# Kernel tuning notes

Measured on AMD Instinct MI355X. Metric: run time of the kernel, lower is better.

The kernel has to match this reference:

```python
import jax, jax.numpy as jnp
import numpy as np


def _dequantize(qweight, scale, zero_point, bits, group_size):
    """Unpack int32-packed weights and apply group-wise dequantization.

    qweight:    [N, K // (32//bits)] int32, value i within an int32 at shift i*bits
    scale/zp:   [N, K // group_size]
    returns W:  [N, K] float32
    """
    vpi = 32 // bits  # values per int32
    mask = (1 << bits) - 1
    N, packed = qweight.shape
    K = packed * vpi
    shifts = (jnp.arange(vpi, dtype=jnp.int32) * bits)  # [vpi]
    # [N, packed, vpi] -> flatten so value i of each int32 lands at consecutive K positions
    q = (qweight[:, :, None] >> shifts[None, None, :]) & mask
    q = q.reshape(N, K // group_size, group_size).astype(jnp.float32)
    w = scale[:, :, None] * (q - zero_point[:, :, None])  # group-wise dequant
    return w.reshape(N, K)


def setup_inputs() -> dict:
    key = jax.random.key(0)
    k1, k2, k3, k4, k5 = jax.random.split(key, 5)
    B, S, K, N = 4, 2048, 4096, 4096
    bits, group_size = 4, 128
    vpi = 32 // bits
    num_groups = K // group_size
    x = jax.random.normal(k1, (B, S, K), dtype=jnp.float32)
    qweight = jax.random.randint(k2, (N, K // vpi), jnp.iinfo(jnp.int32).min,
                                 jnp.iinfo(jnp.int32).max, dtype=jnp.int32)
    scale = jax.random.uniform(k3, (N, num_groups), dtype=jnp.float32,
                               minval=0.001, maxval=0.02)
    zero_point = jax.random.uniform(k4, (N, num_groups), dtype=jnp.float32,
                                    minval=0.0, maxval=float((1 << bits) - 1))
    bias = jax.random.normal(k5, (N,), dtype=jnp.float32)
    return {"x": x, "qweight": qweight, "scale": scale, "zero_point": zero_point,
            "bias": bias, "bits": bits, "group_size": group_size}


def reference(x, qweight, scale, zero_point, bias, bits, group_size):
    # Fused dequant + GEMM: y = x @ W^T + b, W dequantized from packed int4 groups
    w = _dequantize(qweight, scale, zero_point, bits, group_size)  # [N, K]
    y = jnp.einsum('bsk,nk->bsn', x, w)
    return y + bias
```

## Files before the change

### kernel.cpp

```cpp
#include <hip/hip_runtime.h>

#define KD 4096
#define ND 4096
#define GRP 32
#define NT (KD / 64)

typedef unsigned short u16;
typedef float   f32x4  __attribute__((ext_vector_type(4)));
typedef __bf16  bf16x8 __attribute__((ext_vector_type(8)));
typedef unsigned short u16x8 __attribute__((ext_vector_type(8)));
typedef unsigned short u16x4 __attribute__((ext_vector_type(4)));

__device__ __forceinline__ u16 f2bf(float f) {
  unsigned u = __float_as_uint(f);
  return (u16)((u + 0x7fffu + ((u >> 16) & 1u)) >> 16);
}

__device__ __forceinline__ void async16(const void* g, void* l) {
  __builtin_amdgcn_global_load_lds(
      (const __attribute__((address_space(1))) unsigned int*)g,
      (__attribute__((address_space(3))) unsigned int*)l, 16, 0, 0);
}

__global__ __launch_bounds__(256) void prep_kernel(
    const int* __restrict__ qw, const float* __restrict__ scale,
    const float* __restrict__ zp, u16* __restrict__ wout,
    const float4* __restrict__ x, u16x4* __restrict__ xb, int nx) {
  const int nth = gridDim.x * 256;
  const int t0 = blockIdx.x * 256 + threadIdx.x;
  for (int idx = t0; idx < ND * (KD / 8); idx += nth) {
    int n = idx >> 9;
    int p = idx & 511;
    int g = p >> 4;
    float s = scale[n * GRP + g];
    float bz = -s * zp[n * GRP + g];
    unsigned q = (unsigned)qw[idx];
    u16x8 hv;
#pragma unroll
    for (int i = 0; i < 8; ++i)
      hv[i] = f2bf(fmaf((float)((q >> (4 * i)) & 15u), s, bz));
    *(u16x8*)(wout + (size_t)idx * 8) = hv;
  }
  for (int i = t0; i < nx; i += nth) {
    float4 v = x[i];
    u16x4 h;
    h[0] = f2bf(v.x); h[1] = f2bf(v.y); h[2] = f2bf(v.z); h[3] = f2bf(v.w);
    xb[i] = h;
  }
}

__global__ __launch_bounds__(512, 2) void gemm256(
    const u16* __restrict__ xb, const u16* __restrict__ wb,
    const float* __restrict__ bias, float* __restrict__ out) {
  __shared__ u16 As[2][256 * 64];
  __shared__ u16 Bs[2][256 * 64];
  const int tid = threadIdx.x;
  const int l = tid & 63, w = tid >> 6;
  const int wr = w >> 2, wc = w & 3;
  const int col = l & 15, quad = l >> 4, rsw = col & 7;
  const int lr = l >> 3, csrc = (l & 7) ^ lr;

  const int id = blockIdx.y * gridDim.x + blockIdx.x;
  const int nwg = gridDim.x * gridDim.y;
  const int q = nwg >> 3, r = nwg & 7;
  const int xcd = id & 7, off = id >> 3;
  const int wgid = (xcd < r ? xcd * (q + 1) : r * (q + 1) + (xcd - r) * q) + off;
  const int nb = gridDim.x;
  const int m0 = (wgid / nb) * 256;
  const int n0 = (wgid % nb) * 256;

  const u16* asrc = xb + (size_t)(m0 + w * 16 + lr) * KD + csrc * 8;
  const u16* bsrc = wb + (size_t)(n0 + w * 16 + lr) * KD + csrc * 8;

#define STAGE_A(t, h)                                                      \
  do {                                                                     \
    const u16* _g = asrc + (size_t)((h) * 128) * KD + (t) * 64;            \
    u16* _l = &As[(t) & 1][((h) * 128 + w * 16) * 64];                     \
    async16(_g, _l);                                                       \
    async16(_g + (size_t)8 * KD, _l + 8 * 64);                             \
  } while (0)
#define STAGE_B(t, h)                                                      \
  do {                                                                     \
    const u16* _g = bsrc + (size_t)((h) * 128) * KD + (t) * 64;            \
    u16* _l = &Bs[(t) & 1][((h) * 128 + w * 16) * 64];                     \
    async16(_g, _l);                                                       \
    async16(_g + (size_t)8 * KD, _l + 8 * 64);                             \
  } while (0)
#define BAR()   __builtin_amdgcn_s_barrier()
#define SB0()   __builtin_amdgcn_sched_barrier(0)
#define LGKM0() do { asm volatile("s_waitcnt lgkmcnt(0)"); SB0(); } while (0)
#define LDA(Ab, i, kk) \
  (*(const bf16x8*)&(Ab)[(wr * 128 + (i) * 16 + col) * 64 + ((((kk) * 4 + quad) ^ rsw) * 8)])
#define LDB(Bb, j, kk) \
  (*(const bf16x8*)&(Bb)[(wc * 64 + (j) * 16 + col) * 64 + ((((kk) * 4 + quad) ^ rsw) * 8)])

  f32x4 acc[8][4] = {};
  bf16x8 a[4][2], b[4][2];

  STAGE_A(0, 0); STAGE_A(0, 1); STAGE_B(0, 0); STAGE_B(0, 1);
  STAGE_B(1, 0); STAGE_B(1, 1);
  asm volatile("s_waitcnt vmcnt(4)");
  SB0();
  BAR();

  for (int t = 0; t < NT; ++t) {
    const u16* Ab = As[t & 1];
    const u16* Bb = Bs[t & 1];

#pragma unroll
    for (int i = 0; i < 4; ++i) { a[i][0] = LDA(Ab, i, 0); a[i][1] = LDA(Ab, i, 1); }
#pragma unroll
    for (int j = 0; j < 2; ++j) { b[j][0] = LDB(Bb, j, 0); b[j][1] = LDB(Bb, j, 1); }
    if (t + 1 < NT) STAGE_A(t + 1, 0);
    BAR();
    LGKM0();
    __builtin_amdgcn_s_setprio(1);
#pragma unroll
    for (int kk = 0; kk < 2; ++kk)
#pragma unroll
      for (int i = 0; i < 4; ++i)
#pragma unroll
        for (int j = 0; j < 2; ++j)
          acc[i][j] = __builtin_amdgcn_mfma_f32_16x16x32_bf16(a[i][kk], b[j][kk], acc[i][j], 0, 0, 0);
    __builtin_amdgcn_s_setprio(0);
    BAR();

#pragma unroll
    for (int j = 2; j < 4; ++j) { b[j][0] = LDB(Bb, j, 0); b[j][1] = LDB(Bb, j, 1); }
    if (t + 1 < NT) STAGE_A(t + 1, 1);
    BAR();
    LGKM0();
    __builtin_amdgcn_s_setprio(1);
#pragma unroll
    for (int kk = 0; kk < 2; ++kk)
#pragma unroll
      for (int i = 0; i < 4; ++i)
#pragma unroll
        for (int j = 2; j < 4; ++j)
          acc[i][j] = __builtin_amdgcn_mfma_f32_16x16x32_bf16(a[i][kk], b[j][kk], acc[i][j], 0, 0, 0);
    __builtin_amdgcn_s_setprio(0);
    BAR();

#pragma unroll
    for (int i = 0; i < 4; ++i) { a[i][0] = LDA(Ab, i + 4, 0); a[i][1] = LDA(Ab, i + 4, 1); }
    if (t + 2 < NT) STAGE_B(t + 2, 0);
    BAR();
    LGKM0();
    __builtin_amdgcn_s_setprio(1);
#pragma unroll
    for (int kk = 0; kk < 2; ++kk)
#pragma unroll
      for (int i = 0; i < 4; ++i)
#pragma unroll
        for (int j = 0; j < 2; ++j)
          acc[4 + i][j] = __builtin_amdgcn_mfma_f32_16x16x32_bf16(a[i][kk], b[j][kk], acc[4 + i][j], 0, 0, 0);
    __builtin_amdgcn_s_setprio(0);
    BAR();

    if (t + 2 < NT) STAGE_B(t + 2, 1);
    __builtin_amdgcn_s_setprio(1);
#pragma unroll
    for (int kk = 0; kk < 2; ++kk)
#pragma unroll
      for (int i = 0; i < 4; ++i)
#pragma unroll
        for (int j = 2; j < 4; ++j)
          acc[4 + i][j] = __builtin_amdgcn_mfma_f32_16x16x32_bf16(a[i][kk], b[j][kk], acc[4 + i][j], 0, 0, 0);
    __builtin_amdgcn_s_setprio(0);
    if (t + 2 < NT) { asm volatile("s_waitcnt vmcnt(4)"); }
    else            { asm volatile("s_waitcnt vmcnt(0)"); }
    SB0();
    BAR();
    SB0();
  }

#pragma unroll
  for (int j = 0; j < 4; ++j) {
    int n = n0 + wc * 64 + j * 16 + col;
    float bj = bias[n];
#pragma unroll
    for (int i = 0; i < 8; ++i) {
      int mrow = m0 + wr * 128 + i * 16 + quad * 4;
#pragma unroll
      for (int rr = 0; rr < 4; ++rr)
        out[(size_t)(mrow + rr) * ND + n] = acc[i][j][rr] + bj;
    }
  }
#undef STAGE_A
#undef STAGE_B
#undef BAR
#undef SB0
#undef LGKM0
#undef LDA
#undef LDB
}

template <int XF32, int WQ>
__global__ __launch_bounds__(256, 3) void gemm_kernel(
    const u16*   __restrict__ xbp,
    const float* __restrict__ xf,
    const u16*   __restrict__ wbp,
    const int*   __restrict__ qw,
    const float* __restrict__ scale,
    const float* __restrict__ zp,
    const float* __restrict__ bias,
    float* __restrict__ out) {
  __shared__ u16 As[128 * 64];
  __shared__ u16 Bs[128 * 64];
  const int tid = threadIdx.x;
  const int l = tid & 63, w = tid >> 6;
  const int m0 = blockIdx.y * 128, n0 = blockIdx.x * 128;
  const int wm = (w >> 1) * 64, wn = (w & 1) * 64;
  const int col = l & 15, quad = l >> 4;
  const int rsw = col & 7;
  const int lr = l >> 3;
  const int csrc = (l & 7) ^ lr;
  f32x4 acc[4][4] = {};

  for (int k0 = 0; k0 < KD; k0 += 64) {
    __syncthreads();

    if constexpr (XF32) {
#pragma unroll
      for (int it = 0; it < 8; ++it) {
        int fi = it * 256 + tid;
        int row = fi >> 4, cs = fi & 15;
        float4 v = *(const float4*)(xf + (size_t)(m0 + row) * KD + k0 + cs * 4);
        u16x4 h;
        h[0] = f2bf(v.x); h[1] = f2bf(v.y); h[2] = f2bf(v.z); h[3] = f2bf(v.w);
        int slot = (cs >> 1) ^ (row & 7);
        *(u16x4*)(&As[row * 64 + slot * 8 + (cs & 1) * 4]) = h;
      }
    } else {
#pragma unroll
      for (int c = 0; c < 4; ++c) {
        int br = w * 32 + c * 8;
        const u16* g = xbp + (size_t)(m0 + br + lr) * KD + k0 + csrc * 8;
        async16(g, &As[br * 64]);
      }
    }

    if constexpr (WQ) {
#pragma unroll
      for (int it = 0; it < 4; ++it) {
        int qi = it * 256 + tid;
        int row = qi >> 3, p8 = qi & 7;
        int nrow = n0 + row;
        int g = k0 >> 7;
        float s = scale[nrow * GRP + g];
        float bz = -s * zp[nrow * GRP + g];
        unsigned qv = (unsigned)qw[(size_t)nrow * (KD / 8) + (k0 >> 3) + p8];
        u16x8 hv;
#pragma unroll
        for (int i = 0; i < 8; ++i)
          hv[i] = f2bf(fmaf((float)((qv >> (4 * i)) & 15u), s, bz));
        *(u16x8*)(&Bs[row * 64 + ((p8 ^ (row & 7)) * 8)]) = hv;
      }
    } else {
#pragma unroll
      for (int c = 0; c < 4; ++c) {
        int br = w * 32 + c * 8;
        const u16* g = wbp + (size_t)(n0 + br + lr) * KD + k0 + csrc * 8;
        async16(g, &Bs[br * 64]);
      }
    }

    __syncthreads();

#pragma unroll
    for (int kk = 0; kk < 2; ++kk) {
      bf16x8 a[4], b[4];
      const int slot = ((kk * 4 + quad) ^ rsw) * 8;
#pragma unroll
      for (int i = 0; i < 4; ++i)
        a[i] = *(const bf16x8*)&As[(wm + i * 16 + col) * 64 + slot];
#pragma unroll
      for (int j = 0; j < 4; ++j)
        b[j] = *(const bf16x8*)&Bs[(wn + j * 16 + col) * 64 + slot];
#pragma unroll
      for (int i = 0; i < 4; ++i)
#pragma unroll
        for (int j = 0; j < 4; ++j)
          acc[i][j] = __builtin_amdgcn_mfma_f32_16x16x32_bf16(a[i], b[j], acc[i][j], 0, 0, 0);
    }
  }

#pragma unroll
  for (int j = 0; j < 4; ++j) {
    int n = n0 + wn + j * 16 + col;
    float bj = bias[n];
#pragma unroll
    for (int i = 0; i < 4; ++i) {
      int mrow = m0 + wm + i * 16 + quad * 4;
#pragma unroll
      for (int rr = 0; rr < 4; ++rr)
        out[(size_t)(mrow + rr) * ND + n] = acc[i][j][rr] + bj;
    }
  }
}

extern "C" void kernel_launch(void* const* d_in, const int* in_sizes, int n_in,
                              void* d_out, int out_size, void* d_ws, size_t ws_size,
                              hipStream_t stream) {
  const float* x     = (const float*)d_in[0];
  const int*   qw    = (const int*)d_in[1];
  const float* scale = (const float*)d_in[2];
  const float* zp    = (const float*)d_in[3];
  const float* bias  = (const float*)d_in[4];
  float* out = (float*)d_out;

  const int M = in_sizes[0] / KD;

  const size_t needW = (size_t)ND * KD * sizeof(u16);
  const size_t needX = (size_t)M * KD * sizeof(u16);

  if (ws_size >= needW + needX && (M % 256) == 0) {
    u16* wb = (u16*)d_ws;
    u16* xbuf = wb + (size_t)ND * KD;
    prep_kernel<<<2048, 256, 0, stream>>>(qw, scale, zp, wb,
                                          (const float4*)x, (u16x4*)xbuf,
                                          M * (KD / 4));
    dim3 grid(ND / 256, M / 256);
    gemm256<<<grid, dim3(512), 0, stream>>>(xbuf, wb, bias, out);
  } else if (ws_size >= needW) {
    u16* wb = (u16*)d_ws;
    prep_kernel<<<2048, 256, 0, stream>>>(qw, scale, zp, wb, nullptr, nullptr, 0);
    dim3 grid(ND / 128, M / 128);
    gemm_kernel<1, 0><<<grid, dim3(256), 0, stream>>>(nullptr, x, wb, qw, scale, zp, bias, out);
  } else {
    dim3 grid(ND / 128, M / 128);
    gemm_kernel<1, 1><<<grid, dim3(256), 0, stream>>>(nullptr, x, nullptr, qw, scale, zp, bias, out);
  }
}
```

Before: 488.2 us.

## Restructure GEMM pipeline to prefetch A and B two tiles ahead, vectorize prep loads

The main GEMM loop is unrolled by two with a macro, and both A and B tiles are now staged two iterations ahead instead of A one ahead and B two ahead. This moves the A prefetch later in the tile so the global-to-LDS loads have more time to land before they are needed. The loop tail is peeled explicitly with matching vmcnt waits. Separately, the dequant prep kernel now loads int4 vectors of packed weights, so each thread does four times the work per iteration with wider loads. The change puts more loads in flight and makes the wait-count bookkeeping more fragile in exchange for fewer exposed load latencies.

```diff
diff --git a/kernel.cpp b/kernel.cpp
--- a/kernel.cpp
+++ b/kernel.cpp
@@ -28,18 +28,23 @@
     const float4* __restrict__ x, u16x4* __restrict__ xb, int nx) {
   const int nth = gridDim.x * 256;
   const int t0 = blockIdx.x * 256 + threadIdx.x;
-  for (int idx = t0; idx < ND * (KD / 8); idx += nth) {
-    int n = idx >> 9;
-    int p = idx & 511;
-    int g = p >> 4;
+  for (int idx4 = t0; idx4 < ND * (KD / 32); idx4 += nth) {
+    int n = idx4 >> 7;
+    int p4 = idx4 & 127;
+    int g = p4 >> 2;
     float s = scale[n * GRP + g];
     float bz = -s * zp[n * GRP + g];
-    unsigned q = (unsigned)qw[idx];
-    u16x8 hv;
-#pragma unroll
-    for (int i = 0; i < 8; ++i)
-      hv[i] = f2bf(fmaf((float)((q >> (4 * i)) & 15u), s, bz));
-    *(u16x8*)(wout + (size_t)idx * 8) = hv;
+    int4 q4 = ((const int4*)qw)[idx4];
+    const unsigned qv[4] = {(unsigned)q4.x, (unsigned)q4.y,
+                            (unsigned)q4.z, (unsigned)q4.w};
+#pragma unroll
+    for (int k = 0; k < 4; ++k) {
+      u16x8 hv;
+#pragma unroll
+      for (int i = 0; i < 8; ++i)
+        hv[i] = f2bf(fmaf((float)((qv[k] >> (4 * i)) & 15u), s, bz));
+      *(u16x8*)(wout + (size_t)idx4 * 32 + k * 8) = hv;
+    }
   }
   for (int i = t0; i < nx; i += nth) {
     float4 v = x[i];
@@ -93,86 +98,70 @@
   (*(const bf16x8*)&(Ab)[(wr * 128 + (i) * 16 + col) * 64 + ((((kk) * 4 + quad) ^ rsw) * 8)])
 #define LDB(Bb, j, kk) \
   (*(const bf16x8*)&(Bb)[(wc * 64 + (j) * 16 + col) * 64 + ((((kk) * 4 + quad) ^ rsw) * 8)])
+#define MFMA_BLK(IO, JO)                                                   \
+  _Pragma("unroll")                                                        \
+  for (int kk = 0; kk < 2; ++kk)                                           \
+    _Pragma("unroll")                                                      \
+    for (int i = 0; i < 4; ++i)                                            \
+      _Pragma("unroll")                                                    \
+      for (int j = 0; j < 2; ++j)                                          \
+        acc[(IO) + i][(JO) + j] = __builtin_amdgcn_mfma_f32_16x16x32_bf16( \
+            a[i][kk], b[(JO) + j][kk], acc[(IO) + i][(JO) + j], 0, 0, 0);
+#define TILE(Ab, Bb, SB_STMT, SA_STMT, WAIT_STMT)                          \
+  do {                                                                     \
+    _Pragma("unroll")                                                      \
+    for (int i = 0; i < 4; ++i) { a[i][0] = LDA(Ab, i, 0); a[i][1] = LDA(Ab, i, 1); } \
+    _Pragma("unroll")                                                      \
+    for (int j = 0; j < 2; ++j) { b[j][0] = LDB(Bb, j, 0); b[j][1] = LDB(Bb, j, 1); } \
+    BAR(); LGKM0();                                                        \
+    __builtin_amdgcn_s_setprio(1); MFMA_BLK(0, 0);                         \
+    __builtin_amdgcn_s_setprio(0); BAR();                                  \
+    _Pragma("unroll")                                                      \
+    for (int j = 2; j < 4; ++j) { b[j][0] = LDB(Bb, j, 0); b[j][1] = LDB(Bb, j, 1); } \
+    BAR(); LGKM0();                                                        \
+    __builtin_amdgcn_s_setprio(1); MFMA_BLK(0, 2);                         \
+    __builtin_amdgcn_s_setprio(0); BAR();                                  \
+    _Pragma("unroll")                                                      \
+    for (int i = 0; i < 4; ++i) { a[i][0] = LDA(Ab, i + 4, 0); a[i][1] = LDA(Ab, i + 4, 1); } \
+    SB_STMT;                                                               \
+    BAR(); LGKM0();                                                        \
+    __builtin_amdgcn_s_setprio(1); MFMA_BLK(4, 0);                         \
+    __builtin_amdgcn_s_setprio(0); BAR();                                  \
+    SA_STMT;                                                               \
+    __builtin_amdgcn_s_setprio(1); MFMA_BLK(4, 2);                         \
+    __builtin_amdgcn_s_setprio(0);                                         \
+    WAIT_STMT; SB0(); BAR();                                               \
+  } while (0)
 
   f32x4 acc[8][4] = {};
   bf16x8 a[4][2], b[4][2];
 
-  STAGE_A(0, 0); STAGE_A(0, 1); STAGE_B(0, 0); STAGE_B(0, 1);
-  STAGE_B(1, 0); STAGE_B(1, 1);
-  asm volatile("s_waitcnt vmcnt(4)");
+  STAGE_B(0, 0); STAGE_B(0, 1); STAGE_A(0, 0); STAGE_A(0, 1);
+  STAGE_B(1, 0); STAGE_B(1, 1); STAGE_A(1, 0); STAGE_A(1, 1);
+  asm volatile("s_waitcnt vmcnt(8)");
   SB0();
   BAR();
 
-  for (int t = 0; t < NT; ++t) {
-    const u16* Ab = As[t & 1];
-    const u16* Bb = Bs[t & 1];
-
-#pragma unroll
-    for (int i = 0; i < 4; ++i) { a[i][0] = LDA(Ab, i, 0); a[i][1] = LDA(Ab, i, 1); }
-#pragma unroll
-    for (int j = 0; j < 2; ++j) { b[j][0] = LDB(Bb, j, 0); b[j][1] = LDB(Bb, j, 1); }
-    if (t + 1 < NT) STAGE_A(t + 1, 0);
-    BAR();
-    LGKM0();
-    __builtin_amdgcn_s_setprio(1);
-#pragma unroll
-    for (int kk = 0; kk < 2; ++kk)
-#pragma unroll
-      for (int i = 0; i < 4; ++i)
-#pragma unroll
-        for (int j = 0; j < 2; ++j)
-          acc[i][j] = __builtin_amdgcn_mfma_f32_16x16x32_bf16(a[i][kk], b[j][kk], acc[i][j], 0, 0, 0);
-    __builtin_amdgcn_s_setprio(0);
-    BAR();
-
-#pragma unroll
-    for (int j = 2; j < 4; ++j) { b[j][0] = LDB(Bb, j, 0); b[j][1] = LDB(Bb, j, 1); }
-    if (t + 1 < NT) STAGE_A(t + 1, 1);
-    BAR();
-    LGKM0();
-    __builtin_amdgcn_s_setprio(1);
-#pragma unroll
-    for (int kk = 0; kk < 2; ++kk)
-#pragma unroll
-      for (int i = 0; i < 4; ++i)
-#pragma unroll
-        for (int j = 2; j < 4; ++j)
-          acc[i][j] = __builtin_amdgcn_mfma_f32_16x16x32_bf16(a[i][kk], b[j][kk], acc[i][j], 0, 0, 0);
-    __builtin_amdgcn_s_setprio(0);
-    BAR();
-
-#pragma unroll
-    for (int i = 0; i < 4; ++i) { a[i][0] = LDA(Ab, i + 4, 0); a[i][1] = LDA(Ab, i + 4, 1); }
-    if (t + 2 < NT) STAGE_B(t + 2, 0);
-    BAR();
-    LGKM0();
-    __builtin_amdgcn_s_setprio(1);
-#pragma unroll
-    for (int kk = 0; kk < 2; ++kk)
-#pragma unroll
-      for (int i = 0; i < 4; ++i)
-#pragma unroll
-        for (int j = 0; j < 2; ++j)
-          acc[4 + i][j] = __builtin_amdgcn_mfma_f32_16x16x32_bf16(a[i][kk], b[j][kk], acc[4 + i][j], 0, 0, 0);
-    __builtin_amdgcn_s_setprio(0);
-    BAR();
-
-    if (t + 2 < NT) STAGE_B(t + 2, 1);
-    __builtin_amdgcn_s_setprio(1);
-#pragma unroll
-    for (int kk = 0; kk < 2; ++kk)
-#pragma unroll
-      for (int i = 0; i < 4; ++i)
-#pragma unroll
-        for (int j = 2; j < 4; ++j)
-          acc[4 + i][j] = __builtin_amdgcn_mfma_f32_16x16x32_bf16(a[i][kk], b[j][kk], acc[4 + i][j], 0, 0, 0);
-    __builtin_amdgcn_s_setprio(0);
-    if (t + 2 < NT) { asm volatile("s_waitcnt vmcnt(4)"); }
-    else            { asm volatile("s_waitcnt vmcnt(0)"); }
-    SB0();
-    BAR();
-    SB0();
-  }
+  for (int tt = 0; tt < NT - 4; tt += 2) {
+    TILE(As[0], Bs[0],
+         { STAGE_B(tt + 2, 0); STAGE_B(tt + 2, 1); },
+         { STAGE_A(tt + 2, 0); STAGE_A(tt + 2, 1); },
+         asm volatile("s_waitcnt vmcnt(8)"));
+    TILE(As[1], Bs[1],
+         { STAGE_B(tt + 3, 0); STAGE_B(tt + 3, 1); },
+         { STAGE_A(tt + 3, 0); STAGE_A(tt + 3, 1); },
+         asm volatile("s_waitcnt vmcnt(8)"));
+  }
+  TILE(As[0], Bs[0],
+       { STAGE_B(NT - 2, 0); STAGE_B(NT - 2, 1); },
+       { STAGE_A(NT - 2, 0); STAGE_A(NT - 2, 1); },
+       asm volatile("s_waitcnt vmcnt(8)"));
+  TILE(As[1], Bs[1],
+       { STAGE_B(NT - 1, 0); STAGE_B(NT - 1, 1); },
+       { STAGE_A(NT - 1, 0); STAGE_A(NT - 1, 1); },
+       asm volatile("s_waitcnt vmcnt(8)"));
+  TILE(As[0], Bs[0], {;}, {;}, asm volatile("s_waitcnt vmcnt(0)"));
+  TILE(As[1], Bs[1], {;}, {;}, ;);
 
 #pragma unroll
   for (int j = 0; j < 4; ++j) {
@@ -193,6 +182,8 @@
 #undef LGKM0
 #undef LDA
 #undef LDB
+#undef MFMA_BLK
+#undef TILE
 }
 
 template <int XF32, int WQ>
```

Result: faster. 477.7 us (-2.1%).
